# Performance work log

Hardware: AMD Instinct MI355X
Metric: run time of the kernel (lower is better)

Reference implementation:

```python
import jax, jax.numpy as jnp
import numpy as np

N_NODES = 100000
N_EDGES = 1600000
D_IN = 64
D_OUT = 64


def setup_inputs() -> dict:
    key = jax.random.key(0)
    k1, k2, k3 = jax.random.split(key, 3)
    edge_index = jax.random.randint(k1, (2, N_EDGES), 0, N_NODES, dtype=jnp.int64)
    x = jax.random.normal(k2, (N_NODES, D_IN), dtype=jnp.float32)
    W = jax.random.normal(k3, (D_OUT, D_IN), dtype=jnp.float32) * (1.0 / np.sqrt(D_IN))
    return {"edge_index": edge_index, "x": x, "W": W}


def reference(edge_index, x, W):
    # GCN forward: h = W x, then out = D^{-1/2} A D^{-1/2} h (symmetric normalization
    # of the COO edge list, matching normalize_edge_index + CSR SpMM in the original).
    N = x.shape[0]
    row, col = edge_index[0], edge_index[1]
    # degree from row occurrences of the adjacency
    deg = jax.ops.segment_sum(jnp.ones(row.shape, x.dtype), row, num_segments=N)
    dinv_sqrt = jnp.where(deg > 0, 1.0 / jnp.sqrt(deg), 0.0)
    w = dinv_sqrt[row] * dinv_sqrt[col]  # [E] edge weights
    xh = x @ W.T                          # dense linear, bias=False  [N, D_OUT]
    # SpMM: out[r] = sum_e w_e * xh[col_e] for edges with row_e == r
    out = jax.ops.segment_sum(w[:, None] * xh[col], row, num_segments=N)
    return out
```

## Files before the change

### kernel.cpp

```cpp
#include <hip/hip_runtime.h>
#include <hip/hip_fp16.h>

#define D     64
#define RPB   256
#define BCAP  4608
#define EPB   4096
#define NBMAX 400

typedef __attribute__((ext_vector_type(8))) _Float16 f16x8;
typedef __attribute__((ext_vector_type(4))) float    f32x4;

__global__ __launch_bounds__(512) void bucket_kernel(const int* __restrict__ ei, int E,
                                                     int nb,
                                                     int* __restrict__ cursor,
                                                     int* __restrict__ bbuf) {
    __shared__ int hist[NBMAX];
    __shared__ int base_l[NBMAX];
    int tid = threadIdx.x;

    for (int i = tid; i < nb; i += 512) hist[i] = 0;
    __syncthreads();

    int e0 = blockIdx.x * EPB;
    int n  = min(EPB, E - e0);

    for (int idx = tid; idx < n; idx += 512)
        atomicAdd(&hist[ei[e0 + idx] >> 8], 1);
    __syncthreads();

    for (int i = tid; i < nb; i += 512) {
        int c = hist[i];
        base_l[i] = (c > 0) ? atomicAdd(&cursor[i], c) : 0;
        hist[i] = 0;
    }
    __syncthreads();

    for (int idx = tid; idx < n; idx += 512) {
        int r = ei[e0 + idx];
        int c = ei[E + e0 + idx];
        int b = r >> 8;
        int off = base_l[b] + atomicAdd(&hist[b], 1);
        if (off < BCAP)
            bbuf[(size_t)b * BCAP + off] = ((r & (RPB - 1)) << 17) | c;
    }
}

__global__ __launch_bounds__(512) void sort_kernel(const int* __restrict__ cursor,
                                                   int* __restrict__ bbuf,
                                                   float* __restrict__ dinv,
                                                   int4* __restrict__ rowinfo, int N) {
    __shared__ int sorted[BCAP];
    __shared__ int hist[RPB];
    __shared__ int curs[RPB];
    __shared__ int wsum[4];
    int b = blockIdx.x, tid = threadIdx.x;
    int cnt = min(cursor[b], BCAP);
    int* gbuf = bbuf + (size_t)b * BCAP;

    if (tid < RPB) hist[tid] = 0;
    __syncthreads();
    for (int j = tid; j < cnt; j += 512) atomicAdd(&hist[gbuf[j] >> 17], 1);
    __syncthreads();

    int dv = 0, s = 0;
    if (tid < RPB) {
        dv = hist[tid];
        s = dv;
#pragma unroll
        for (int off = 1; off < 64; off <<= 1) {
            int t = __shfl_up(s, off);
            if ((tid & 63) >= off) s += t;
        }
        if ((tid & 63) == 63) wsum[tid >> 6] = s;
    }
    __syncthreads();
    if (tid < RPB) {
        int woff = 0;
#pragma unroll
        for (int i = 0; i < 3; ++i)
            if ((tid >> 6) > i) woff += wsum[i];
        int excl = s + woff - dv;
        int r = (b << 8) + tid;
        if (r < N) {
            float di = (dv > 0) ? rsqrtf((float)dv) : 0.0f;
            dinv[r] = di;
            rowinfo[r] = make_int4(b * BCAP + excl, dv, __float_as_int(di), 0);
        }
        curs[tid] = excl;
    }
    __syncthreads();

    for (int j = tid; j < cnt; j += 512) {
        int v = gbuf[j];
        int pos = atomicAdd(&curs[v >> 17], 1);
        sorted[pos] = v;
    }
    __syncthreads();
    for (int j = tid; j < cnt; j += 512) gbuf[j] = sorted[j];
}

__global__ __launch_bounds__(256) void linear_kernel(const float* __restrict__ x,
                                                     const float* __restrict__ W,
                                                     const float* __restrict__ dinv,
                                                     __half* __restrict__ xh, int M) {
    int tid  = threadIdx.x;
    int lane = tid & 63;
    int wv   = tid >> 6;
    int r16  = lane & 15;
    int quad = lane >> 4;

    if (blockIdx.x == 0 && tid < D) xh[(size_t)M * D + tid] = __float2half(0.0f);

    f16x8 Bf[4][2];
#pragma unroll
    for (int g = 0; g < 4; ++g)
#pragma unroll
        for (int s = 0; s < 2; ++s) {
            const float4* wp = (const float4*)(W + (size_t)(16 * g + r16) * D + 32 * s + quad * 8);
            float4 w0 = wp[0], w1 = wp[1];
            f16x8 h;
            h[0] = (_Float16)w0.x; h[1] = (_Float16)w0.y;
            h[2] = (_Float16)w0.z; h[3] = (_Float16)w0.w;
            h[4] = (_Float16)w1.x; h[5] = (_Float16)w1.y;
            h[6] = (_Float16)w1.z; h[7] = (_Float16)w1.w;
            Bf[g][s] = h;
        }

    int ntiles = (M + 15) / 16;
    int stride = gridDim.x * 4;
    for (int t = blockIdx.x * 4 + wv; t < ntiles; t += stride) {
        int r0 = t * 16;
        int ra = min(r0 + r16, M - 1);
        const float4* xp = (const float4*)(x + (size_t)ra * D + quad * 8);
        float4 a0 = xp[0], a1 = xp[1], a2 = xp[8], a3 = xp[9];
        f16x8 A0, A1;
        A0[0] = (_Float16)a0.x; A0[1] = (_Float16)a0.y; A0[2] = (_Float16)a0.z; A0[3] = (_Float16)a0.w;
        A0[4] = (_Float16)a1.x; A0[5] = (_Float16)a1.y; A0[6] = (_Float16)a1.z; A0[7] = (_Float16)a1.w;
        A1[0] = (_Float16)a2.x; A1[1] = (_Float16)a2.y; A1[2] = (_Float16)a2.z; A1[3] = (_Float16)a2.w;
        A1[4] = (_Float16)a3.x; A1[5] = (_Float16)a3.y; A1[6] = (_Float16)a3.z; A1[7] = (_Float16)a3.w;

        f32x4 acc[4];
#pragma unroll
        for (int g = 0; g < 4; ++g) {
            f32x4 z = {0.f, 0.f, 0.f, 0.f};
            z = __builtin_amdgcn_mfma_f32_16x16x32_f16(A0, Bf[g][0], z, 0, 0, 0);
            acc[g] = __builtin_amdgcn_mfma_f32_16x16x32_f16(A1, Bf[g][1], z, 0, 0, 0);
        }

#pragma unroll
        for (int reg = 0; reg < 4; ++reg) {
            int rr = r0 + quad * 4 + reg;
            if (rr < M) {
                float dvr = dinv[rr];
                __half* op = xh + (size_t)rr * D + r16;
#pragma unroll
                for (int g = 0; g < 4; ++g)
                    op[16 * g] = __float2half(dvr * acc[g][reg]);
            }
        }
    }
}

__global__ __launch_bounds__(256) void spmm_kernel(const int4* __restrict__ rowinfo,
                                                   const int* __restrict__ bbuf,
                                                   const __half2* __restrict__ xh2,
                                                   float2* __restrict__ out2,
                                                   int N, int stride) {
    int wid = (blockIdx.x * 256 + threadIdx.x) >> 6;
    int c   = threadIdx.x & 63;
    int sub = c >> 5;
    int f   = c & 31;

    int r0 = wid;
    if (r0 >= N) return;

    int4 ri0 = rowinfo[r0];
    int4 ri1 = (r0 + stride < N) ? rowinfo[r0 + stride] : make_int4(0, 0, 0, 0);
    int  cn0 = (c < min(ri0.y, 64)) ? (bbuf[ri0.x + c] & 0x1FFFF) : N;

    for (int r = r0; r < N; r += stride) {
        int rn  = r + stride;
        int rn2 = rn + stride;
        int4 ri2 = (rn2 < N) ? rowinfo[rn2] : make_int4(0, 0, 0, 0);
        int  cn1 = (rn < N && c < min(ri1.y, 64)) ? (bbuf[ri1.x + c] & 0x1FFFF) : N;

        int   d  = ri0.y;
        float dr = __int_as_float(ri0.z);
        float ax = 0.f, ay = 0.f;

        int n = min(d, 64);
        int n16 = (n + 15) & ~15;
        for (int k = 0; k < n16; k += 16) {
            int e0 = __shfl(cn0, k +  0 + sub);
            int e1 = __shfl(cn0, k +  2 + sub);
            int e2 = __shfl(cn0, k +  4 + sub);
            int e3 = __shfl(cn0, k +  6 + sub);
            int e4 = __shfl(cn0, k +  8 + sub);
            int e5 = __shfl(cn0, k + 10 + sub);
            int e6 = __shfl(cn0, k + 12 + sub);
            int e7 = __shfl(cn0, k + 14 + sub);
            float2 v0 = __half22float2(xh2[(size_t)e0 * 32 + f]);
            float2 v1 = __half22float2(xh2[(size_t)e1 * 32 + f]);
            float2 v2 = __half22float2(xh2[(size_t)e2 * 32 + f]);
            float2 v3 = __half22float2(xh2[(size_t)e3 * 32 + f]);
            float2 v4 = __half22float2(xh2[(size_t)e4 * 32 + f]);
            float2 v5 = __half22float2(xh2[(size_t)e5 * 32 + f]);
            float2 v6 = __half22float2(xh2[(size_t)e6 * 32 + f]);
            float2 v7 = __half22float2(xh2[(size_t)e7 * 32 + f]);
            ax += ((v0.x + v1.x) + (v2.x + v3.x)) + ((v4.x + v5.x) + (v6.x + v7.x));
            ay += ((v0.y + v1.y) + (v2.y + v3.y)) + ((v4.y + v5.y) + (v6.y + v7.y));
        }
        for (int j0 = 64; j0 < d; j0 += 64) {
            int nn = min(d - j0, 64);
            int cnx = (c < nn) ? (bbuf[ri0.x + j0 + c] & 0x1FFFF) : N;
            int m16 = (nn + 15) & ~15;
            for (int k = 0; k < m16; k += 16) {
                int e0 = __shfl(cnx, k +  0 + sub);
                int e1 = __shfl(cnx, k +  2 + sub);
                int e2 = __shfl(cnx, k +  4 + sub);
                int e3 = __shfl(cnx, k +  6 + sub);
                int e4 = __shfl(cnx, k +  8 + sub);
                int e5 = __shfl(cnx, k + 10 + sub);
                int e6 = __shfl(cnx, k + 12 + sub);
                int e7 = __shfl(cnx, k + 14 + sub);
                float2 v0 = __half22float2(xh2[(size_t)e0 * 32 + f]);
                float2 v1 = __half22float2(xh2[(size_t)e1 * 32 + f]);
                float2 v2 = __half22float2(xh2[(size_t)e2 * 32 + f]);
                float2 v3 = __half22float2(xh2[(size_t)e3 * 32 + f]);
                float2 v4 = __half22float2(xh2[(size_t)e4 * 32 + f]);
                float2 v5 = __half22float2(xh2[(size_t)e5 * 32 + f]);
                float2 v6 = __half22float2(xh2[(size_t)e6 * 32 + f]);
                float2 v7 = __half22float2(xh2[(size_t)e7 * 32 + f]);
                ax += ((v0.x + v1.x) + (v2.x + v3.x)) + ((v4.x + v5.x) + (v6.x + v7.x));
                ay += ((v0.y + v1.y) + (v2.y + v3.y)) + ((v4.y + v5.y) + (v6.y + v7.y));
            }
        }

        float sx = ax + __shfl(ax, c ^ 32);
        float sy = ay + __shfl(ay, c ^ 32);
        if (sub == 0) {
            float2 res = make_float2(dr * sx, dr * sy);
            __builtin_nontemporal_store(__builtin_bit_cast(double, res),
                                        (double*)&out2[(size_t)r * 32 + f]);
        }
        ri0 = ri1; ri1 = ri2; cn0 = cn1;
    }
}

extern "C" void kernel_launch(void* const* d_in, const int* in_sizes, int n_in,
                              void* d_out, int out_size, void* d_ws, size_t ws_size,
                              hipStream_t stream) {
    const int*   ei = (const int*)d_in[0];
    const float* x  = (const float*)d_in[1];
    const float* W  = (const float*)d_in[2];
    float* out = (float*)d_out;

    int E  = in_sizes[0] / 2;
    int N  = in_sizes[1] / D;
    int nb = (N + RPB - 1) / RPB;

    char* p = (char*)d_ws;
    size_t off = 0;
    auto take = [&](size_t bytes) -> char* {
        char* cur = p + off;
        off = (off + bytes + 255) & ~(size_t)255;
        return cur;
    };
    float*  dinv    = (float*)take((size_t)N * 4);
    int4*   rowinfo = (int4*)take((size_t)N * 16);
    int*    cursor  = (int*)take((size_t)nb * 4);
    int*    bbuf    = (int*)take((size_t)nb * BCAP * 4);
    __half* xh      = (__half*)take((size_t)(N + 1) * D * 2);
    (void)ws_size;

    hipMemsetAsync(cursor, 0, (size_t)nb * 4, stream);

    bucket_kernel<<<(E + EPB - 1) / EPB, 512, 0, stream>>>(ei, E, nb, cursor, bbuf);
    sort_kernel<<<nb, 512, 0, stream>>>(cursor, bbuf, dinv, rowinfo, N);
    linear_kernel<<<1024, 256, 0, stream>>>(x, W, dinv, xh, N);

    int spmm_blocks = 3072;
    spmm_kernel<<<spmm_blocks, 256, 0, stream>>>(rowinfo, bbuf, (const __half2*)xh,
                                                 (float2*)out, N, spmm_blocks * 4);
}
```

Baseline: 164.7 us.

## Fuse per-bucket sort into SpMM with LDS-staged weighted edges and smaller buckets

The separate sort and SpMM kernels are merged. Each block counting-sorts its bucket of edges into shared memory as (col, dinv[col]) pairs and then aggregates the rows directly from shared memory. The linear kernel no longer scales by dinv. A separate degree kernel computes dinv before the fused kernel, bucket size drops to 128 rows, and the cursor array is padded to avoid atomic contention. This removes the global write-back of sorted edges and the rowinfo array, but gives up the persistent grid-stride prefetching of the old SpMM and uses one block per 128 rows with large LDS use.

```diff
diff --git a/kernel.cpp b/kernel.cpp
--- a/kernel.cpp
+++ b/kernel.cpp
@@ -1,107 +1,18 @@
 #include <hip/hip_runtime.h>
 #include <hip/hip_fp16.h>
 
-#define D     64
-#define RPB   256
-#define BCAP  4608
-#define EPB   4096
-#define NBMAX 400
+#define D      64
+#define RPB    128
+#define BCAP   2432
+#define EPB    4096
+#define NBMAX  800
+#define CSTRIDE 16
 
 typedef __attribute__((ext_vector_type(8))) _Float16 f16x8;
 typedef __attribute__((ext_vector_type(4))) float    f32x4;
 
-__global__ __launch_bounds__(512) void bucket_kernel(const int* __restrict__ ei, int E,
-                                                     int nb,
-                                                     int* __restrict__ cursor,
-                                                     int* __restrict__ bbuf) {
-    __shared__ int hist[NBMAX];
-    __shared__ int base_l[NBMAX];
-    int tid = threadIdx.x;
-
-    for (int i = tid; i < nb; i += 512) hist[i] = 0;
-    __syncthreads();
-
-    int e0 = blockIdx.x * EPB;
-    int n  = min(EPB, E - e0);
-
-    for (int idx = tid; idx < n; idx += 512)
-        atomicAdd(&hist[ei[e0 + idx] >> 8], 1);
-    __syncthreads();
-
-    for (int i = tid; i < nb; i += 512) {
-        int c = hist[i];
-        base_l[i] = (c > 0) ? atomicAdd(&cursor[i], c) : 0;
-        hist[i] = 0;
-    }
-    __syncthreads();
-
-    for (int idx = tid; idx < n; idx += 512) {
-        int r = ei[e0 + idx];
-        int c = ei[E + e0 + idx];
-        int b = r >> 8;
-        int off = base_l[b] + atomicAdd(&hist[b], 1);
-        if (off < BCAP)
-            bbuf[(size_t)b * BCAP + off] = ((r & (RPB - 1)) << 17) | c;
-    }
-}
-
-__global__ __launch_bounds__(512) void sort_kernel(const int* __restrict__ cursor,
-                                                   int* __restrict__ bbuf,
-                                                   float* __restrict__ dinv,
-                                                   int4* __restrict__ rowinfo, int N) {
-    __shared__ int sorted[BCAP];
-    __shared__ int hist[RPB];
-    __shared__ int curs[RPB];
-    __shared__ int wsum[4];
-    int b = blockIdx.x, tid = threadIdx.x;
-    int cnt = min(cursor[b], BCAP);
-    int* gbuf = bbuf + (size_t)b * BCAP;
-
-    if (tid < RPB) hist[tid] = 0;
-    __syncthreads();
-    for (int j = tid; j < cnt; j += 512) atomicAdd(&hist[gbuf[j] >> 17], 1);
-    __syncthreads();
-
-    int dv = 0, s = 0;
-    if (tid < RPB) {
-        dv = hist[tid];
-        s = dv;
-#pragma unroll
-        for (int off = 1; off < 64; off <<= 1) {
-            int t = __shfl_up(s, off);
-            if ((tid & 63) >= off) s += t;
-        }
-        if ((tid & 63) == 63) wsum[tid >> 6] = s;
-    }
-    __syncthreads();
-    if (tid < RPB) {
-        int woff = 0;
-#pragma unroll
-        for (int i = 0; i < 3; ++i)
-            if ((tid >> 6) > i) woff += wsum[i];
-        int excl = s + woff - dv;
-        int r = (b << 8) + tid;
-        if (r < N) {
-            float di = (dv > 0) ? rsqrtf((float)dv) : 0.0f;
-            dinv[r] = di;
-            rowinfo[r] = make_int4(b * BCAP + excl, dv, __float_as_int(di), 0);
-        }
-        curs[tid] = excl;
-    }
-    __syncthreads();
-
-    for (int j = tid; j < cnt; j += 512) {
-        int v = gbuf[j];
-        int pos = atomicAdd(&curs[v >> 17], 1);
-        sorted[pos] = v;
-    }
-    __syncthreads();
-    for (int j = tid; j < cnt; j += 512) gbuf[j] = sorted[j];
-}
-
 __global__ __launch_bounds__(256) void linear_kernel(const float* __restrict__ x,
                                                      const float* __restrict__ W,
-                                                     const float* __restrict__ dinv,
                                                      __half* __restrict__ xh, int M) {
     int tid  = threadIdx.x;
     int lane = tid & 63;
@@ -151,99 +62,171 @@
         for (int reg = 0; reg < 4; ++reg) {
             int rr = r0 + quad * 4 + reg;
             if (rr < M) {
-                float dvr = dinv[rr];
                 __half* op = xh + (size_t)rr * D + r16;
 #pragma unroll
                 for (int g = 0; g < 4; ++g)
-                    op[16 * g] = __float2half(dvr * acc[g][reg]);
+                    op[16 * g] = __float2half(acc[g][reg]);
             }
         }
     }
 }
 
-__global__ __launch_bounds__(256) void spmm_kernel(const int4* __restrict__ rowinfo,
-                                                   const int* __restrict__ bbuf,
-                                                   const __half2* __restrict__ xh2,
-                                                   float2* __restrict__ out2,
-                                                   int N, int stride) {
-    int wid = (blockIdx.x * 256 + threadIdx.x) >> 6;
-    int c   = threadIdx.x & 63;
-    int sub = c >> 5;
-    int f   = c & 31;
-
-    int r0 = wid;
-    if (r0 >= N) return;
-
-    int4 ri0 = rowinfo[r0];
-    int4 ri1 = (r0 + stride < N) ? rowinfo[r0 + stride] : make_int4(0, 0, 0, 0);
-    int  cn0 = (c < min(ri0.y, 64)) ? (bbuf[ri0.x + c] & 0x1FFFF) : N;
-
-    for (int r = r0; r < N; r += stride) {
-        int rn  = r + stride;
-        int rn2 = rn + stride;
-        int4 ri2 = (rn2 < N) ? rowinfo[rn2] : make_int4(0, 0, 0, 0);
-        int  cn1 = (rn < N && c < min(ri1.y, 64)) ? (bbuf[ri1.x + c] & 0x1FFFF) : N;
-
-        int   d  = ri0.y;
-        float dr = __int_as_float(ri0.z);
+__global__ __launch_bounds__(512) void bucket_kernel(const int* __restrict__ ei, int E,
+                                                     int nb,
+                                                     int* __restrict__ cursor,
+                                                     int* __restrict__ bbuf) {
+    __shared__ int hist[NBMAX];
+    __shared__ int base_l[NBMAX];
+    int tid = threadIdx.x;
+
+    for (int i = tid; i < nb; i += 512) hist[i] = 0;
+    __syncthreads();
+
+    int e0 = blockIdx.x * EPB;
+    int n  = min(EPB, E - e0);
+
+    for (int idx = tid; idx < n; idx += 512)
+        atomicAdd(&hist[ei[e0 + idx] >> 7], 1);
+    __syncthreads();
+
+    for (int i = tid; i < nb; i += 512) {
+        int c = hist[i];
+        base_l[i] = (c > 0) ? atomicAdd(&cursor[i * CSTRIDE], c) : 0;
+        hist[i] = 0;
+    }
+    __syncthreads();
+
+    for (int idx = tid; idx < n; idx += 512) {
+        int r = ei[e0 + idx];
+        int c = ei[E + e0 + idx];
+        int b = r >> 7;
+        int off = base_l[b] + atomicAdd(&hist[b], 1);
+        if (off < BCAP)
+            bbuf[(size_t)b * BCAP + off] = ((r & (RPB - 1)) << 17) | c;
+    }
+}
+
+__global__ __launch_bounds__(256) void deg_kernel(const int* __restrict__ cursor,
+                                                  const int* __restrict__ bbuf,
+                                                  float* __restrict__ dinv, int N) {
+    __shared__ int h[RPB];
+    int b = blockIdx.x, tid = threadIdx.x;
+    if (tid < RPB) h[tid] = 0;
+    __syncthreads();
+    int cnt = min(cursor[b * CSTRIDE], BCAP);
+    const int* gbuf = bbuf + (size_t)b * BCAP;
+    for (int j = tid; j < cnt; j += 256) atomicAdd(&h[gbuf[j] >> 17], 1);
+    __syncthreads();
+    if (tid < RPB) {
+        int r = (b << 7) + tid;
+        if (r < N) {
+            int d = h[tid];
+            dinv[r] = (d > 0) ? rsqrtf((float)d) : 0.0f;
+        }
+    }
+}
+
+__global__ __launch_bounds__(512) void sortspmm_kernel(const int* __restrict__ cursor,
+                                                       const int* __restrict__ bbuf,
+                                                       const float* __restrict__ dinv,
+                                                       const __half2* __restrict__ xh2,
+                                                       float2* __restrict__ out2, int N) {
+    __shared__ int2 sw[BCAP];
+    __shared__ int  deg_s[RPB];
+    __shared__ int  excl_s[RPB];
+    __shared__ int  curs_s[RPB];
+    __shared__ int  wsum[2];
+
+    int b = blockIdx.x, tid = threadIdx.x;
+    int cnt = min(cursor[b * CSTRIDE], BCAP);
+    const int* gbuf = bbuf + (size_t)b * BCAP;
+
+    if (tid < RPB) deg_s[tid] = 0;
+    __syncthreads();
+    for (int j = tid; j < cnt; j += 512) atomicAdd(&deg_s[gbuf[j] >> 17], 1);
+    __syncthreads();
+
+    int dv = 0, s = 0;
+    if (tid < RPB) {
+        dv = deg_s[tid];
+        s = dv;
+#pragma unroll
+        for (int off = 1; off < 64; off <<= 1) {
+            int t = __shfl_up(s, off);
+            if ((tid & 63) >= off) s += t;
+        }
+        if ((tid & 63) == 63) wsum[tid >> 6] = s;
+    }
+    __syncthreads();
+    if (tid < RPB) {
+        int excl = s - dv + (((tid >> 6) == 1) ? wsum[0] : 0);
+        excl_s[tid] = excl;
+        curs_s[tid] = excl;
+    }
+    __syncthreads();
+
+    for (int j = tid; j < cnt; j += 512) {
+        int v  = gbuf[j];
+        int cn = v & 0x1FFFF;
+        float w = dinv[cn];
+        int pos = atomicAdd(&curs_s[v >> 17], 1);
+        sw[pos] = make_int2(cn, __float_as_int(w));
+    }
+    __syncthreads();
+
+    int lane = tid & 63;
+    int wave = tid >> 6;
+    int sub  = lane >> 5;
+    int f    = lane & 31;
+
+    for (int rl = wave; rl < RPB; rl += 8) {
+        int r = (b << 7) + rl;
+        if (r >= N) continue;
+        int d  = deg_s[rl];
+        int s0 = excl_s[rl];
+        float dr = (d > 0) ? rsqrtf((float)d) : 0.0f;
+
         float ax = 0.f, ay = 0.f;
-
-        int n = min(d, 64);
-        int n16 = (n + 15) & ~15;
-        for (int k = 0; k < n16; k += 16) {
-            int e0 = __shfl(cn0, k +  0 + sub);
-            int e1 = __shfl(cn0, k +  2 + sub);
-            int e2 = __shfl(cn0, k +  4 + sub);
-            int e3 = __shfl(cn0, k +  6 + sub);
-            int e4 = __shfl(cn0, k +  8 + sub);
-            int e5 = __shfl(cn0, k + 10 + sub);
-            int e6 = __shfl(cn0, k + 12 + sub);
-            int e7 = __shfl(cn0, k + 14 + sub);
-            float2 v0 = __half22float2(xh2[(size_t)e0 * 32 + f]);
-            float2 v1 = __half22float2(xh2[(size_t)e1 * 32 + f]);
-            float2 v2 = __half22float2(xh2[(size_t)e2 * 32 + f]);
-            float2 v3 = __half22float2(xh2[(size_t)e3 * 32 + f]);
-            float2 v4 = __half22float2(xh2[(size_t)e4 * 32 + f]);
-            float2 v5 = __half22float2(xh2[(size_t)e5 * 32 + f]);
-            float2 v6 = __half22float2(xh2[(size_t)e6 * 32 + f]);
-            float2 v7 = __half22float2(xh2[(size_t)e7 * 32 + f]);
-            ax += ((v0.x + v1.x) + (v2.x + v3.x)) + ((v4.x + v5.x) + (v6.x + v7.x));
-            ay += ((v0.y + v1.y) + (v2.y + v3.y)) + ((v4.y + v5.y) + (v6.y + v7.y));
-        }
-        for (int j0 = 64; j0 < d; j0 += 64) {
-            int nn = min(d - j0, 64);
-            int cnx = (c < nn) ? (bbuf[ri0.x + j0 + c] & 0x1FFFF) : N;
-            int m16 = (nn + 15) & ~15;
+        for (int j0 = 0; j0 < d; j0 += 64) {
+            int m = min(d - j0, 64);
+            int m16 = (m + 15) & ~15;
+            int base = s0 + j0;
             for (int k = 0; k < m16; k += 16) {
-                int e0 = __shfl(cnx, k +  0 + sub);
-                int e1 = __shfl(cnx, k +  2 + sub);
-                int e2 = __shfl(cnx, k +  4 + sub);
-                int e3 = __shfl(cnx, k +  6 + sub);
-                int e4 = __shfl(cnx, k +  8 + sub);
-                int e5 = __shfl(cnx, k + 10 + sub);
-                int e6 = __shfl(cnx, k + 12 + sub);
-                int e7 = __shfl(cnx, k + 14 + sub);
-                float2 v0 = __half22float2(xh2[(size_t)e0 * 32 + f]);
-                float2 v1 = __half22float2(xh2[(size_t)e1 * 32 + f]);
-                float2 v2 = __half22float2(xh2[(size_t)e2 * 32 + f]);
-                float2 v3 = __half22float2(xh2[(size_t)e3 * 32 + f]);
-                float2 v4 = __half22float2(xh2[(size_t)e4 * 32 + f]);
-                float2 v5 = __half22float2(xh2[(size_t)e5 * 32 + f]);
-                float2 v6 = __half22float2(xh2[(size_t)e6 * 32 + f]);
-                float2 v7 = __half22float2(xh2[(size_t)e7 * 32 + f]);
-                ax += ((v0.x + v1.x) + (v2.x + v3.x)) + ((v4.x + v5.x) + (v6.x + v7.x));
-                ay += ((v0.y + v1.y) + (v2.y + v3.y)) + ((v4.y + v5.y) + (v6.y + v7.y));
+                int i0 = k +  0 + sub, i1 = k +  2 + sub, i2 = k +  4 + sub, i3 = k +  6 + sub;
+                int i4 = k +  8 + sub, i5 = k + 10 + sub, i6 = k + 12 + sub, i7 = k + 14 + sub;
+                int2 p0 = (i0 < m) ? sw[base + i0] : make_int2(N, 0);
+                int2 p1 = (i1 < m) ? sw[base + i1] : make_int2(N, 0);
+                int2 p2 = (i2 < m) ? sw[base + i2] : make_int2(N, 0);
+                int2 p3 = (i3 < m) ? sw[base + i3] : make_int2(N, 0);
+                int2 p4 = (i4 < m) ? sw[base + i4] : make_int2(N, 0);
+                int2 p5 = (i5 < m) ? sw[base + i5] : make_int2(N, 0);
+                int2 p6 = (i6 < m) ? sw[base + i6] : make_int2(N, 0);
+                int2 p7 = (i7 < m) ? sw[base + i7] : make_int2(N, 0);
+                float2 v0 = __half22float2(xh2[(size_t)p0.x * 32 + f]);
+                float2 v1 = __half22float2(xh2[(size_t)p1.x * 32 + f]);
+                float2 v2 = __half22float2(xh2[(size_t)p2.x * 32 + f]);
+                float2 v3 = __half22float2(xh2[(size_t)p3.x * 32 + f]);
+                float2 v4 = __half22float2(xh2[(size_t)p4.x * 32 + f]);
+                float2 v5 = __half22float2(xh2[(size_t)p5.x * 32 + f]);
+                float2 v6 = __half22float2(xh2[(size_t)p6.x * 32 + f]);
+                float2 v7 = __half22float2(xh2[(size_t)p7.x * 32 + f]);
+                ax = fmaf(__int_as_float(p0.y), v0.x, ax); ay = fmaf(__int_as_float(p0.y), v0.y, ay);
+                ax = fmaf(__int_as_float(p1.y), v1.x, ax); ay = fmaf(__int_as_float(p1.y), v1.y, ay);
+                ax = fmaf(__int_as_float(p2.y), v2.x, ax); ay = fmaf(__int_as_float(p2.y), v2.y, ay);
+                ax = fmaf(__int_as_float(p3.y), v3.x, ax); ay = fmaf(__int_as_float(p3.y), v3.y, ay);
+                ax = fmaf(__int_as_float(p4.y), v4.x, ax); ay = fmaf(__int_as_float(p4.y), v4.y, ay);
+                ax = fmaf(__int_as_float(p5.y), v5.x, ax); ay = fmaf(__int_as_float(p5.y), v5.y, ay);
+                ax = fmaf(__int_as_float(p6.y), v6.x, ax); ay = fmaf(__int_as_float(p6.y), v6.y, ay);
+                ax = fmaf(__int_as_float(p7.y), v7.x, ax); ay = fmaf(__int_as_float(p7.y), v7.y, ay);
             }
         }
-
-        float sx = ax + __shfl(ax, c ^ 32);
-        float sy = ay + __shfl(ay, c ^ 32);
+        float sx = ax + __shfl(ax, lane ^ 32);
+        float sy = ay + __shfl(ay, lane ^ 32);
         if (sub == 0) {
             float2 res = make_float2(dr * sx, dr * sy);
             __builtin_nontemporal_store(__builtin_bit_cast(double, res),
                                         (double*)&out2[(size_t)r * 32 + f]);
         }
-        ri0 = ri1; ri1 = ri2; cn0 = cn1;
     }
 }
 
@@ -266,20 +249,17 @@
         off = (off + bytes + 255) & ~(size_t)255;
         return cur;
     };
-    float*  dinv    = (float*)take((size_t)N * 4);
-    int4*   rowinfo = (int4*)take((size_t)N * 16);
-    int*    cursor  = (int*)take((size_t)nb * 4);
-    int*    bbuf    = (int*)take((size_t)nb * BCAP * 4);
-    __half* xh      = (__half*)take((size_t)(N + 1) * D * 2);
+    float*  dinv   = (float*)take((size_t)N * 4);
+    int*    cursor = (int*)take((size_t)nb * CSTRIDE * 4);
+    int*    bbuf   = (int*)take((size_t)nb * BCAP * 4);
+    __half* xh     = (__half*)take((size_t)(N + 1) * D * 2);
     (void)ws_size;
 
-    hipMemsetAsync(cursor, 0, (size_t)nb * 4, stream);
-
+    hipMemsetAsync(cursor, 0, (size_t)nb * CSTRIDE * 4, stream);
+
+    linear_kernel<<<1024, 256, 0, stream>>>(x, W, xh, N);
     bucket_kernel<<<(E + EPB - 1) / EPB, 512, 0, stream>>>(ei, E, nb, cursor, bbuf);
-    sort_kernel<<<nb, 512, 0, stream>>>(cursor, bbuf, dinv, rowinfo, N);
-    linear_kernel<<<1024, 256, 0, stream>>>(x, W, dinv, xh, N);
-
-    int spmm_blocks = 3072;
-    spmm_kernel<<<spmm_blocks, 256, 0, stream>>>(rowinfo, bbuf, (const __half2*)xh,
-                                                 (float2*)out, N, spmm_blocks * 4);
-}
+    deg_kernel<<<nb, 256, 0, stream>>>(cursor, bbuf, dinv, N);
+    sortspmm_kernel<<<nb, 512, 0, stream>>>(cursor, bbuf, dinv,
+                                            (const __half2*)xh, (float2*)out, N);
+}
```

After: 183.5 us. 1.11x slower.
